# Kernel optimization log

Hardware: AMD Instinct MI355X
Metric: run time of the kernel (lower is better)

## Reference

```python
import jax, jax.numpy as jnp
import numpy as np
from jax import lax

BATCH, HID = 8192, 512


def setup_inputs() -> dict:
    key = jax.random.key(0)
    ks = jax.random.split(key, 9)
    s = 0.05
    return {
        "h": jax.random.normal(ks[0], (BATCH, HID), jnp.float32),
        "W1": jax.random.normal(ks[1], (2 * HID, HID), jnp.float32) * s,
        "b1": jax.random.normal(ks[2], (2 * HID,), jnp.float32) * s,
        "W2": jax.random.normal(ks[3], (2 * HID, 2 * HID), jnp.float32) * s,
        "b2": jax.random.normal(ks[4], (2 * HID,), jnp.float32) * s,
        "W3": jax.random.normal(ks[5], (HID, 2 * HID), jnp.float32) * s,
        "b3": jax.random.normal(ks[6], (HID,), jnp.float32) * s,
        "Wt": jax.random.normal(ks[7], (HID, 1), jnp.float32) * s,
        "bt": jax.random.normal(ks[8], (HID,), jnp.float32) * s,
        "n_steps": 10,
    }


def reference(h, W1, b1, W2, b2, W3, b3, Wt, bt, n_steps):
    dt = 1.0 / n_steps  # t_span = (0, 1)

    def ode_func(t, hh):
        # time_embed(Linear(1,H)) on a column of t's: t * Wt[:,0] + bt
        t_emb = t * Wt[:, 0] + bt                      # (H,), broadcast over batch
        x = hh + t_emb                                 # (B, H)
        x = jnp.tanh(x @ W1.T + b1)                    # (B, 2H)
        x = jnp.tanh(x @ W2.T + b2)                    # (B, 2H)
        return x @ W3.T + b3                           # (B, H)

    def rk4_step(hh, t):
        k1 = ode_func(t, hh)
        k2 = ode_func(t + dt / 2, hh + dt / 2 * k1)
        k3 = ode_func(t + dt / 2, hh + dt / 2 * k2)
        k4 = ode_func(t + dt, hh + dt * k3)
        return hh + dt / 6 * (k1 + 2 * k2 + 2 * k3 + k4), None

    ts = (jnp.arange(n_steps, dtype=h.dtype) * dt)     # step start times
    h_out, _ = lax.scan(rk4_step, h, ts)
    return h_out
```

## Files before the change

### kernel.cpp

```cpp
#include <hip/hip_runtime.h>
#include <hip/hip_bf16.h>
#include <math.h>
#include <stdint.h>

using bf16 = __hip_bfloat16;
typedef __attribute__((ext_vector_type(8))) short short8;
typedef __attribute__((ext_vector_type(4))) float floatx4;
typedef __attribute__((ext_vector_type(4))) int int4v;

typedef const __attribute__((address_space(1))) void* gptr_t;
typedef __attribute__((address_space(3))) void* lptr_t;

__device__ __forceinline__ void load_lds16(const void* g, void* l) {
    __builtin_amdgcn_global_load_lds((gptr_t)(uintptr_t)g, (lptr_t)(uintptr_t)l, 16, 0, 0);
}

#define WAIT_VM(n) __builtin_amdgcn_s_waitcnt(0x0F70 | ((n) & 15) | (((n) >> 4) << 14))

__device__ __forceinline__ float fast_tanh(float x) {
    float e = __expf(2.f * x);
    return 1.f - 2.f / (e + 1.f);
}


__global__ void __launch_bounds__(256, 2)
gemm_tanh4(const bf16* __restrict__ A, const bf16* __restrict__ W,
           const float* __restrict__ bias, int8_t* __restrict__ out,
           int K, int N) {
    constexpr int MT = 4, NT = 4;
    __shared__ alignas(16) bf16 lA[2][128 * 64];
    __shared__ alignas(16) bf16 lB[2][128 * 64];

    const int b   = blockIdx.x + gridDim.x * blockIdx.y;
    const int xcd = b & 7, j = b >> 3;
    const int bx  = j & 7;
    const int by  = xcd + 8 * (j >> 3);

    const int tid  = threadIdx.x;
    const int lane = tid & 63;
    const int w    = tid >> 6;
    const int wr   = w >> 1, wc = w & 1;
    const int quad = lane >> 4, l16 = lane & 15;
    const int brow = by * 128;
    const int bcol = bx * 128;

    const bf16* gA[4]; const bf16* gW[4]; int lq[4];
#pragma unroll
    for (int jj = 0; jj < 4; ++jj) {
        const int q = tid + jj * 256;
        const int r = q >> 3, s = (q & 7) ^ (r & 7);
        gA[jj] = A + (size_t)(brow + r) * K + s * 8;
        gW[jj] = W + (size_t)(bcol + r) * K + s * 8;
        lq[jj] = q * 8;
    }

    floatx4 acc[MT][NT];
    const floatx4 zero = {0.f, 0.f, 0.f, 0.f};
#pragma unroll
    for (int mt = 0; mt < MT; ++mt)
#pragma unroll
        for (int nt = 0; nt < NT; ++nt) acc[mt][nt] = zero;

    const int arow0 = wr * 64 + l16;
    const int brow0 = wc * 64 + l16;
    const int x7 = l16 & 7;

    const int nIter = K / 64;
#pragma unroll
    for (int jj = 0; jj < 4; ++jj) load_lds16(gA[jj], &lA[0][0] + lq[jj]);
#pragma unroll
    for (int jj = 0; jj < 4; ++jj) load_lds16(gW[jj], &lB[0][0] + lq[jj]);

    for (int kt = 0; kt < nIter; ++kt) {
        const int cur = kt & 1;
        if (kt + 1 < nIter) {
#pragma unroll
            for (int jj = 0; jj < 4; ++jj)
                load_lds16(gA[jj] + (kt + 1) * 64, &lA[cur ^ 1][0] + lq[jj]);
#pragma unroll
            for (int jj = 0; jj < 4; ++jj)
                load_lds16(gW[jj] + (kt + 1) * 64, &lB[cur ^ 1][0] + lq[jj]);
            WAIT_VM(8);
        } else {
            WAIT_VM(0);
        }
        __builtin_amdgcn_s_barrier();

#pragma unroll
        for (int kk = 0; kk < 2; ++kk) {
            const int sw = ((kk * 4 + quad) ^ x7) * 8;
            short8 af[MT], bfr[NT];
#pragma unroll
            for (int mt = 0; mt < MT; ++mt)
                af[mt] = *(const short8*)(&lA[cur][0] + (arow0 + mt * 16) * 64 + sw);
#pragma unroll
            for (int nt = 0; nt < NT; ++nt)
                bfr[nt] = *(const short8*)(&lB[cur][0] + (brow0 + nt * 16) * 64 + sw);
#pragma unroll
            for (int mt = 0; mt < MT; ++mt)
#pragma unroll
                for (int nt = 0; nt < NT; ++nt)
                    acc[mt][nt] = __builtin_amdgcn_mfma_f32_16x16x32_bf16(
                        af[mt], bfr[nt], acc[mt][nt], 0, 0, 0);
        }
        __builtin_amdgcn_s_barrier();
    }

    const int m0 = brow + wr * 64 + quad * 4;
    const int n0 = bcol + wc * 64 + l16;
#pragma unroll
    for (int mt = 0; mt < MT; ++mt)
#pragma unroll
        for (int nt = 0; nt < NT; ++nt) {
            const int n = n0 + nt * 16;
            const float bb = bias[n];
#pragma unroll
            for (int i = 0; i < 4; ++i) {
                const int m = m0 + mt * 16 + i;
                const float t = fast_tanh(acc[mt][nt][i] + bb);
                out[(size_t)m * N + n] = (int8_t)__float2int_rn(t * 127.f);
            }
        }
}

__global__ void __launch_bounds__(256, 2)
gemm_tanh_i8(const int8_t* __restrict__ A, const int8_t* __restrict__ W,
             const float* __restrict__ dq, const float* __restrict__ bias,
             int8_t* __restrict__ out, int K, int N) {
    constexpr int MT = 4, NT = 4;
    __shared__ alignas(16) int8_t lA[2][128 * 128];
    __shared__ alignas(16) int8_t lB[2][128 * 128];

    const int b   = blockIdx.x + gridDim.x * blockIdx.y;
    const int xcd = b & 7, j = b >> 3;
    const int bx  = j & 7;
    const int by  = xcd + 8 * (j >> 3);

    const int tid  = threadIdx.x;
    const int lane = tid & 63;
    const int w    = tid >> 6;
    const int wr   = w >> 1, wc = w & 1;
    const int quad = lane >> 4, l16 = lane & 15;
    const int brow = by * 128;
    const int bcol = bx * 128;

    const int8_t* gA[4]; const int8_t* gW[4]; int lq[4];
#pragma unroll
    for (int jj = 0; jj < 4; ++jj) {
        const int q = tid + jj * 256;
        const int r = q >> 3, s = (q & 7) ^ (r & 7);
        gA[jj] = A + (size_t)(brow + r) * K + s * 16;
        gW[jj] = W + (size_t)(bcol + r) * K + s * 16;
        lq[jj] = q * 16;
    }

    int4v acc[MT][NT];
    const int4v izero = {0, 0, 0, 0};
#pragma unroll
    for (int mt = 0; mt < MT; ++mt)
#pragma unroll
        for (int nt = 0; nt < NT; ++nt) acc[mt][nt] = izero;

    const int arow0 = wr * 64 + l16;
    const int brow0 = wc * 64 + l16;
    const int x7 = l16 & 7;

    const int nIter = K / 128;
#pragma unroll
    for (int jj = 0; jj < 4; ++jj) load_lds16(gA[jj], &lA[0][0] + lq[jj]);
#pragma unroll
    for (int jj = 0; jj < 4; ++jj) load_lds16(gW[jj], &lB[0][0] + lq[jj]);

    for (int kt = 0; kt < nIter; ++kt) {
        const int cur = kt & 1;
        if (kt + 1 < nIter) {
#pragma unroll
            for (int jj = 0; jj < 4; ++jj)
                load_lds16(gA[jj] + (kt + 1) * 128, &lA[cur ^ 1][0] + lq[jj]);
#pragma unroll
            for (int jj = 0; jj < 4; ++jj)
                load_lds16(gW[jj] + (kt + 1) * 128, &lB[cur ^ 1][0] + lq[jj]);
            WAIT_VM(8);
        } else {
            WAIT_VM(0);
        }
        __builtin_amdgcn_s_barrier();

#pragma unroll
        for (int kk = 0; kk < 2; ++kk) {
            const int sw = ((kk * 4 + quad) ^ x7) * 16;
            int4v af[MT], bfr[NT];
#pragma unroll
            for (int mt = 0; mt < MT; ++mt)
                af[mt] = *(const int4v*)(&lA[cur][(arow0 + mt * 16) * 128 + sw]);
#pragma unroll
            for (int nt = 0; nt < NT; ++nt)
                bfr[nt] = *(const int4v*)(&lB[cur][(brow0 + nt * 16) * 128 + sw]);
#pragma unroll
            for (int mt = 0; mt < MT; ++mt)
#pragma unroll
                for (int nt = 0; nt < NT; ++nt)
                    acc[mt][nt] = __builtin_amdgcn_mfma_i32_16x16x64_i8(
                        af[mt], bfr[nt], acc[mt][nt], 0, 0, 0);
        }
        __builtin_amdgcn_s_barrier();
    }

    const int m0 = brow + wr * 64 + quad * 4;
    const int n0 = bcol + wc * 64 + l16;
#pragma unroll
    for (int mt = 0; mt < MT; ++mt)
#pragma unroll
        for (int nt = 0; nt < NT; ++nt) {
            const int n = n0 + nt * 16;
            const float bb = bias[n];
            const float dqn = dq[n];
#pragma unroll
            for (int i = 0; i < 4; ++i) {
                const int m = m0 + mt * 16 + i;
                const float t = fast_tanh((float)acc[mt][nt][i] * dqn + bb);
                out[(size_t)m * N + n] = (int8_t)__float2int_rn(t * 127.f);
            }
        }
}

__global__ void __launch_bounds__(256, 2)
gemm_k(const int8_t* __restrict__ A, const int8_t* __restrict__ W,
       const float* __restrict__ dq, const float* __restrict__ bias, int K,
       bf16* __restrict__ kacc, const bf16* __restrict__ hb_src,
       const float* __restrict__ h_src, float* __restrict__ h_out,
       bf16* __restrict__ hb_out, bf16* __restrict__ x0_out,
       const float* __restrict__ temb, float alpha, float dt6, int mode) {
    constexpr int MT = 4, NT = 2;
    __shared__ alignas(16) int8_t lA[2][128 * 128];
    __shared__ alignas(16) int8_t lB[2][64 * 128];

    const int b   = blockIdx.x + gridDim.x * blockIdx.y;
    const int xcd = b & 7, j = b >> 3;
    const int bx  = j & 7;
    const int by  = xcd + 8 * (j >> 3);

    const int tid  = threadIdx.x;
    const int lane = tid & 63;
    const int w    = tid >> 6;
    const int wr   = w >> 1, wc = w & 1;
    const int quad = lane >> 4, l16 = lane & 15;
    const int brow = by * 128;
    const int bcol = bx * 64;

    const int8_t* gA[4]; int lqA[4];
    const int8_t* gW[2]; int lqB[2];
#pragma unroll
    for (int jj = 0; jj < 4; ++jj) {
        const int q = tid + jj * 256;
        const int r = q >> 3, s = (q & 7) ^ (r & 7);
        gA[jj]  = A + (size_t)(brow + r) * K + s * 16;
        lqA[jj] = q * 16;
    }
#pragma unroll
    for (int jj = 0; jj < 2; ++jj) {
        const int q = tid + jj * 256;
        const int r = q >> 3, s = (q & 7) ^ (r & 7);
        gW[jj]  = W + (size_t)(bcol + r) * K + s * 16;
        lqB[jj] = q * 16;
    }

    int4v acc[MT][NT];
    const int4v izero = {0, 0, 0, 0};
#pragma unroll
    for (int mt = 0; mt < MT; ++mt)
#pragma unroll
        for (int nt = 0; nt < NT; ++nt) acc[mt][nt] = izero;

    const int arow0 = wr * 64 + l16;
    const int brow0 = wc * 32 + l16;
    const int x7 = l16 & 7;

    const int nIter = K / 128;
#pragma unroll
    for (int jj = 0; jj < 4; ++jj) load_lds16(gA[jj], &lA[0][0] + lqA[jj]);
#pragma unroll
    for (int jj = 0; jj < 2; ++jj) load_lds16(gW[jj], &lB[0][0] + lqB[jj]);

    for (int kt = 0; kt < nIter; ++kt) {
        const int cur = kt & 1;
        if (kt + 1 < nIter) {
#pragma unroll
            for (int jj = 0; jj < 4; ++jj)
                load_lds16(gA[jj] + (kt + 1) * 128, &lA[cur ^ 1][0] + lqA[jj]);
#pragma unroll
            for (int jj = 0; jj < 2; ++jj)
                load_lds16(gW[jj] + (kt + 1) * 128, &lB[cur ^ 1][0] + lqB[jj]);
            WAIT_VM(6);
        } else {
            WAIT_VM(0);
        }
        __builtin_amdgcn_s_barrier();

#pragma unroll
        for (int kk = 0; kk < 2; ++kk) {
            const int sw = ((kk * 4 + quad) ^ x7) * 16;
            int4v af[MT], bfr[NT];
#pragma unroll
            for (int mt = 0; mt < MT; ++mt)
                af[mt] = *(const int4v*)(&lA[cur][(arow0 + mt * 16) * 128 + sw]);
#pragma unroll
            for (int nt = 0; nt < NT; ++nt)
                bfr[nt] = *(const int4v*)(&lB[cur][(brow0 + nt * 16) * 128 + sw]);
#pragma unroll
            for (int mt = 0; mt < MT; ++mt)
#pragma unroll
                for (int nt = 0; nt < NT; ++nt)
                    acc[mt][nt] = __builtin_amdgcn_mfma_i32_16x16x64_i8(
                        af[mt], bfr[nt], acc[mt][nt], 0, 0, 0);
        }
        __builtin_amdgcn_s_barrier();
    }

    const int m0 = brow + wr * 64 + quad * 4;
    const int n0 = bcol + wc * 32 + l16;
#pragma unroll
    for (int mt = 0; mt < MT; ++mt)
#pragma unroll
        for (int nt = 0; nt < NT; ++nt) {
            const int n = n0 + nt * 16;
            const float bb = bias[n];
            const float dqn = dq[n];
            const float te = temb[n];
#pragma unroll
            for (int i = 0; i < 4; ++i) {
                const int m = m0 + mt * 16 + i;
                const size_t idx = (size_t)m * 512 + n;
                const float kv = (float)acc[mt][nt][i] * dqn + bb;
                if (mode == 0) {
                    kacc[idx] = __float2bfloat16(kv);
                    x0_out[idx] = __float2bfloat16(
                        __bfloat162float(hb_src[idx]) + alpha * kv + te);
                } else if (mode == 1) {
                    kacc[idx] = __float2bfloat16(__bfloat162float(kacc[idx]) + 2.f * kv);
                    x0_out[idx] = __float2bfloat16(
                        __bfloat162float(hb_src[idx]) + alpha * kv + te);
                } else {
                    const float hn = h_src[idx] + dt6 * (__bfloat162float(kacc[idx]) + kv);
                    h_out[idx] = hn;
                    hb_out[idx] = __float2bfloat16(hn);
                    if (x0_out) x0_out[idx] = __float2bfloat16(hn + te);
                }
            }
        }
}

__global__ void f2b_kern(const float* __restrict__ src, bf16* __restrict__ dst, int n) {
    const int i = blockIdx.x * blockDim.x + threadIdx.x;
    if (i < n) dst[i] = __float2bfloat16(src[i]);
}

__global__ void quantW_row(const float* __restrict__ W, int K,
                           int8_t* __restrict__ out, float* __restrict__ dq) {
    __shared__ float red[256];
    const int row = blockIdx.x, tid = threadIdx.x;
    const float* src = W + (size_t)row * K;
    float m = 0.f;
    for (int k = tid; k < K; k += 256) m = fmaxf(m, fabsf(src[k]));
    red[tid] = m;
    __syncthreads();
    for (int s = 128; s > 0; s >>= 1) {
        if (tid < s) red[tid] = fmaxf(red[tid], red[tid + s]);
        __syncthreads();
    }
    const float rmax = fmaxf(red[0], 1e-8f);
    const float sc = 127.f / rmax;
    int8_t* dst = out + (size_t)row * K;
    for (int k = tid; k < K; k += 256) {
        int v = __float2int_rn(src[k] * sc);
        v = v > 127 ? 127 : (v < -127 ? -127 : v);
        dst[k] = (int8_t)v;
    }
    if (tid == 0) dq[row] = rmax / (127.f * 127.f);
}

__global__ void temb_kern(const float* __restrict__ Wt, const float* __restrict__ bt,
                          float* __restrict__ temb, float half_dt, int total) {
    const int i = blockIdx.x * blockDim.x + threadIdx.x;
    if (i < total) {
        const int j = i >> 9, n = i & 511;
        temb[i] = (j * half_dt) * Wt[n] + bt[n];
    }
}

__global__ void prep_kern(const float* __restrict__ h, const float* __restrict__ temb0,
                          bf16* __restrict__ x0, bf16* __restrict__ hb, int total) {
    const int i = blockIdx.x * blockDim.x + threadIdx.x;
    if (i < total) {
        const float hv = h[i];
        x0[i] = __float2bfloat16(hv + temb0[i & 511]);
        hb[i] = __float2bfloat16(hv);
    }
}

extern "C" void kernel_launch(void* const* d_in, const int* in_sizes, int n_in,
                              void* d_out, int out_size, void* d_ws, size_t ws_size,
                              hipStream_t stream) {
    const float* h_in = (const float*)d_in[0];
    const float* W1 = (const float*)d_in[1];
    const float* b1 = (const float*)d_in[2];
    const float* W2 = (const float*)d_in[3];
    const float* b2 = (const float*)d_in[4];
    const float* W3 = (const float*)d_in[5];
    const float* b3 = (const float*)d_in[6];
    const float* Wt = (const float*)d_in[7];
    const float* bt = (const float*)d_in[8];
    const int B = 8192, H = 512, H2 = 1024, NS = 10;
    const float dt = 1.f / NS;

    char* ws = (char*)d_ws;
    auto alloc = [&](size_t bytes) {
        char* p = ws;
        ws += (bytes + 255) & ~(size_t)255;
        return p;
    };
    bf16* W1b = (bf16*)alloc((size_t)H2 * H * 2);
    int8_t* W2i = (int8_t*)alloc((size_t)H2 * H2);
    float* dq2  = (float*)alloc((size_t)H2 * 4);
    int8_t* W3i = (int8_t*)alloc((size_t)H * H2);
    float* dq3  = (float*)alloc((size_t)H * 4);
    bf16* x0b = (bf16*)alloc((size_t)B * H * 2);
    int8_t* x1i = (int8_t*)alloc((size_t)B * H2);
    int8_t* x2i = (int8_t*)alloc((size_t)B * H2);
    bf16* kacc = (bf16*)alloc((size_t)B * H * 2);
    bf16* hb   = (bf16*)alloc((size_t)B * H * 2);
    float* temb = (float*)alloc((size_t)21 * H * 4);
    float* hbuf = (float*)d_out;

    {
        int n = H2 * H;
        f2b_kern<<<(n + 255) / 256, 256, 0, stream>>>(W1, W1b, n);
        quantW_row<<<H2, 256, 0, stream>>>(W2, H2, W2i, dq2);
        quantW_row<<<H, 256, 0, stream>>>(W3, H2, W3i, dq3);
    }
    {
        const int total = 21 * H;
        temb_kern<<<(total + 255) / 256, 256, 0, stream>>>(Wt, bt, temb, dt * 0.5f, total);
    }
    {
        const int total = B * H;
        prep_kern<<<(total + 255) / 256, 256, 0, stream>>>(h_in, temb, x0b, hb, total);
    }

    const dim3 blk256(256);
    const dim3 g12(H2 / 128, B / 128);
    const dim3 g3(H / 64, B / 128);

    for (int s = 0; s < NS; ++s) {
        const float* hs = (s == 0) ? h_in : hbuf;
        const float* tmid = temb + (size_t)(2 * s + 1) * H;
        const float* tend = temb + (size_t)(2 * s + 2) * H;
        for (int e = 0; e < 4; ++e) {
            gemm_tanh4<<<g12, blk256, 0, stream>>>(x0b, W1b, b1, x1i, H, H2);
            gemm_tanh_i8<<<g12, blk256, 0, stream>>>(x1i, W2i, dq2, b2, x2i, H2, H2);
            if (e == 0)
                gemm_k<<<g3, blk256, 0, stream>>>(x2i, W3i, dq3, b3, H2, kacc, hb, hs,
                                                  nullptr, nullptr, x0b, tmid,
                                                  dt * 0.5f, 0.f, 0);
            else if (e == 1)
                gemm_k<<<g3, blk256, 0, stream>>>(x2i, W3i, dq3, b3, H2, kacc, hb, hs,
                                                  nullptr, nullptr, x0b, tmid,
                                                  dt * 0.5f, 0.f, 1);
            else if (e == 2)
                gemm_k<<<g3, blk256, 0, stream>>>(x2i, W3i, dq3, b3, H2, kacc, hb, hs,
                                                  nullptr, nullptr, x0b, tend,
                                                  dt, 0.f, 1);
            else
                gemm_k<<<g3, blk256, 0, stream>>>(x2i, W3i, dq3, b3, H2, kacc, hb, hs,
                                                  hbuf, hb,
                                                  (s == NS - 1) ? nullptr : x0b,
                                                  tend, 0.f, dt / 6.f, 2);
        }
    }
}
```

Measured before the change: 2.103 ms.

## Fold W3 into W1 and track pre-activation h·W1 across RK4 stages

The change precomputes W13 = W1·W3 and folds the time embedding and the biases into per-stage constant tables. It then keeps h·W1ᵀ as a float state, so each RK4 stage is an int8 layer-2 GEMM followed by a fused W13 GEMM that directly produces the next layer-1 activation. The separate layer-1 GEMM per stage and the bf16 state round-trips go away. The k accumulation is kept as int16 sums of quantized tanh outputs, and one combined update GEMM advances both hW1 and h. The cost is extra float hW1 traffic, and numerical error rises from int8 quantization of the composed W13 and from the k-average being quantized to int8.

```diff
diff --git a/kernel.cpp b/kernel.cpp
--- a/kernel.cpp
+++ b/kernel.cpp
@@ -24,9 +24,9 @@
 
 
 __global__ void __launch_bounds__(256, 2)
-gemm_tanh4(const bf16* __restrict__ A, const bf16* __restrict__ W,
-           const float* __restrict__ bias, int8_t* __restrict__ out,
-           int K, int N) {
+gemm_init(const bf16* __restrict__ A, const bf16* __restrict__ W,
+          const float* __restrict__ c0n, float* __restrict__ hW1,
+          int8_t* __restrict__ x1q, int K) {
     constexpr int MT = 4, NT = 4;
     __shared__ alignas(16) bf16 lA[2][128 * 64];
     __shared__ alignas(16) bf16 lB[2][128 * 64];
@@ -113,21 +113,24 @@
 #pragma unroll
         for (int nt = 0; nt < NT; ++nt) {
             const int n = n0 + nt * 16;
-            const float bb = bias[n];
+            const float cn = c0n[n];
 #pragma unroll
             for (int i = 0; i < 4; ++i) {
                 const int m = m0 + mt * 16 + i;
-                const float t = fast_tanh(acc[mt][nt][i] + bb);
-                out[(size_t)m * N + n] = (int8_t)__float2int_rn(t * 127.f);
+                const size_t idx = (size_t)m * 1024 + n;
+                const float v = acc[mt][nt][i];
+                hW1[idx] = v;
+                x1q[idx] = (int8_t)__float2int_rn(127.f * fast_tanh(v + cn));
             }
         }
 }
 
 __global__ void __launch_bounds__(256, 2)
-gemm_tanh_i8(const int8_t* __restrict__ A, const int8_t* __restrict__ W,
-             const float* __restrict__ dq, const float* __restrict__ bias,
-             int8_t* __restrict__ out, int K, int N) {
-    constexpr int MT = 4, NT = 4;
+gemm_l2(const int8_t* __restrict__ A, const int8_t* __restrict__ W,
+        const float* __restrict__ dq, const float* __restrict__ bias,
+        int8_t* __restrict__ x2q, int16_t* __restrict__ xacc16,
+        int8_t* __restrict__ xaccq, int mode) {
+    constexpr int MT = 4, NT = 4, K = 1024;
     __shared__ alignas(16) int8_t lA[2][128 * 128];
     __shared__ alignas(16) int8_t lB[2][128 * 128];
 
@@ -218,22 +221,30 @@
 #pragma unroll
             for (int i = 0; i < 4; ++i) {
                 const int m = m0 + mt * 16 + i;
-                const float t = fast_tanh((float)acc[mt][nt][i] * dqn + bb);
-                out[(size_t)m * N + n] = (int8_t)__float2int_rn(t * 127.f);
+                const size_t idx = (size_t)m * 1024 + n;
+                const int q = __float2int_rn(
+                    127.f * fast_tanh((float)acc[mt][nt][i] * dqn + bb));
+                if (mode == 0) {
+                    x2q[idx] = (int8_t)q;
+                    xacc16[idx] = (int16_t)q;
+                } else if (mode == 1) {
+                    x2q[idx] = (int8_t)q;
+                    xacc16[idx] = (int16_t)(xacc16[idx] + 2 * q);
+                } else {
+                    const int tot = (int)xacc16[idx] + q;
+                    xaccq[idx] = (int8_t)__float2int_rn((float)tot * (1.f / 6.f));
+                }
             }
         }
 }
 
 __global__ void __launch_bounds__(256, 2)
-gemm_k(const int8_t* __restrict__ A, const int8_t* __restrict__ W,
-       const float* __restrict__ dq, const float* __restrict__ bias, int K,
-       bf16* __restrict__ kacc, const bf16* __restrict__ hb_src,
-       const float* __restrict__ h_src, float* __restrict__ h_out,
-       bf16* __restrict__ hb_out, bf16* __restrict__ x0_out,
-       const float* __restrict__ temb, float alpha, float dt6, int mode) {
-    constexpr int MT = 4, NT = 2;
+gemm_u(const int8_t* __restrict__ A, const int8_t* __restrict__ W,
+       const float* __restrict__ dq, const float* __restrict__ hW1,
+       const float* __restrict__ c, float alpha, int8_t* __restrict__ x1q) {
+    constexpr int MT = 4, NT = 4, K = 1024;
     __shared__ alignas(16) int8_t lA[2][128 * 128];
-    __shared__ alignas(16) int8_t lB[2][64 * 128];
+    __shared__ alignas(16) int8_t lB[2][128 * 128];
 
     const int b   = blockIdx.x + gridDim.x * blockIdx.y;
     const int xcd = b & 7, j = b >> 3;
@@ -246,23 +257,16 @@
     const int wr   = w >> 1, wc = w & 1;
     const int quad = lane >> 4, l16 = lane & 15;
     const int brow = by * 128;
-    const int bcol = bx * 64;
-
-    const int8_t* gA[4]; int lqA[4];
-    const int8_t* gW[2]; int lqB[2];
+    const int bcol = bx * 128;
+
+    const int8_t* gA[4]; const int8_t* gW[4]; int lq[4];
 #pragma unroll
     for (int jj = 0; jj < 4; ++jj) {
         const int q = tid + jj * 256;
         const int r = q >> 3, s = (q & 7) ^ (r & 7);
-        gA[jj]  = A + (size_t)(brow + r) * K + s * 16;
-        lqA[jj] = q * 16;
-    }
-#pragma unroll
-    for (int jj = 0; jj < 2; ++jj) {
-        const int q = tid + jj * 256;
-        const int r = q >> 3, s = (q & 7) ^ (r & 7);
-        gW[jj]  = W + (size_t)(bcol + r) * K + s * 16;
-        lqB[jj] = q * 16;
+        gA[jj] = A + (size_t)(brow + r) * K + s * 16;
+        gW[jj] = W + (size_t)(bcol + r) * K + s * 16;
+        lq[jj] = q * 16;
     }
 
     int4v acc[MT][NT];
@@ -273,25 +277,25 @@
         for (int nt = 0; nt < NT; ++nt) acc[mt][nt] = izero;
 
     const int arow0 = wr * 64 + l16;
-    const int brow0 = wc * 32 + l16;
+    const int brow0 = wc * 64 + l16;
     const int x7 = l16 & 7;
 
     const int nIter = K / 128;
 #pragma unroll
-    for (int jj = 0; jj < 4; ++jj) load_lds16(gA[jj], &lA[0][0] + lqA[jj]);
-#pragma unroll
-    for (int jj = 0; jj < 2; ++jj) load_lds16(gW[jj], &lB[0][0] + lqB[jj]);
+    for (int jj = 0; jj < 4; ++jj) load_lds16(gA[jj], &lA[0][0] + lq[jj]);
+#pragma unroll
+    for (int jj = 0; jj < 4; ++jj) load_lds16(gW[jj], &lB[0][0] + lq[jj]);
 
     for (int kt = 0; kt < nIter; ++kt) {
         const int cur = kt & 1;
         if (kt + 1 < nIter) {
 #pragma unroll
             for (int jj = 0; jj < 4; ++jj)
-                load_lds16(gA[jj] + (kt + 1) * 128, &lA[cur ^ 1][0] + lqA[jj]);
-#pragma unroll
-            for (int jj = 0; jj < 2; ++jj)
-                load_lds16(gW[jj] + (kt + 1) * 128, &lB[cur ^ 1][0] + lqB[jj]);
-            WAIT_VM(6);
+                load_lds16(gA[jj] + (kt + 1) * 128, &lA[cur ^ 1][0] + lq[jj]);
+#pragma unroll
+            for (int jj = 0; jj < 4; ++jj)
+                load_lds16(gW[jj] + (kt + 1) * 128, &lB[cur ^ 1][0] + lq[jj]);
+            WAIT_VM(8);
         } else {
             WAIT_VM(0);
         }
@@ -318,41 +322,164 @@
     }
 
     const int m0 = brow + wr * 64 + quad * 4;
-    const int n0 = bcol + wc * 32 + l16;
+    const int n0 = bcol + wc * 64 + l16;
 #pragma unroll
     for (int mt = 0; mt < MT; ++mt)
 #pragma unroll
         for (int nt = 0; nt < NT; ++nt) {
             const int n = n0 + nt * 16;
-            const float bb = bias[n];
-            const float dqn = dq[n];
-            const float te = temb[n];
+            const float dqa = dq[n] * alpha;
+            const float cn = c[n];
 #pragma unroll
             for (int i = 0; i < 4; ++i) {
                 const int m = m0 + mt * 16 + i;
-                const size_t idx = (size_t)m * 512 + n;
-                const float kv = (float)acc[mt][nt][i] * dqn + bb;
-                if (mode == 0) {
-                    kacc[idx] = __float2bfloat16(kv);
-                    x0_out[idx] = __float2bfloat16(
-                        __bfloat162float(hb_src[idx]) + alpha * kv + te);
-                } else if (mode == 1) {
-                    kacc[idx] = __float2bfloat16(__bfloat162float(kacc[idx]) + 2.f * kv);
-                    x0_out[idx] = __float2bfloat16(
-                        __bfloat162float(hb_src[idx]) + alpha * kv + te);
+                const size_t idx = (size_t)m * 1024 + n;
+                const float u = hW1[idx] + dqa * (float)acc[mt][nt][i] + cn;
+                x1q[idx] = (int8_t)__float2int_rn(127.f * fast_tanh(u));
+            }
+        }
+}
+
+__global__ void __launch_bounds__(256, 2)
+gemm_upd(const int8_t* __restrict__ A, const int8_t* __restrict__ W,
+         const float* __restrict__ dq, const float* __restrict__ updc,
+         float dtv, float* __restrict__ hW1, const float* __restrict__ c0n,
+         int8_t* __restrict__ x1q, const float* __restrict__ hsrc,
+         float* __restrict__ hdst, int last, int bxoff) {
+    constexpr int MT = 4, NT = 4, K = 1024;
+    __shared__ alignas(16) int8_t lA[2][128 * 128];
+    __shared__ alignas(16) int8_t lB[2][128 * 128];
+
+    const int bx = blockIdx.x + bxoff;
+    const int by = blockIdx.y;
+
+    const int tid  = threadIdx.x;
+    const int lane = tid & 63;
+    const int w    = tid >> 6;
+    const int wr   = w >> 1, wc = w & 1;
+    const int quad = lane >> 4, l16 = lane & 15;
+    const int brow = by * 128;
+    const int bcol = bx * 128;
+
+    const int8_t* gA[4]; const int8_t* gW[4]; int lq[4];
+#pragma unroll
+    for (int jj = 0; jj < 4; ++jj) {
+        const int q = tid + jj * 256;
+        const int r = q >> 3, s = (q & 7) ^ (r & 7);
+        gA[jj] = A + (size_t)(brow + r) * K + s * 16;
+        gW[jj] = W + (size_t)(bcol + r) * K + s * 16;
+        lq[jj] = q * 16;
+    }
+
+    int4v acc[MT][NT];
+    const int4v izero = {0, 0, 0, 0};
+#pragma unroll
+    for (int mt = 0; mt < MT; ++mt)
+#pragma unroll
+        for (int nt = 0; nt < NT; ++nt) acc[mt][nt] = izero;
+
+    const int arow0 = wr * 64 + l16;
+    const int brow0 = wc * 64 + l16;
+    const int x7 = l16 & 7;
+
+    const int nIter = K / 128;
+#pragma unroll
+    for (int jj = 0; jj < 4; ++jj) load_lds16(gA[jj], &lA[0][0] + lq[jj]);
+#pragma unroll
+    for (int jj = 0; jj < 4; ++jj) load_lds16(gW[jj], &lB[0][0] + lq[jj]);
+
+    for (int kt = 0; kt < nIter; ++kt) {
+        const int cur = kt & 1;
+        if (kt + 1 < nIter) {
+#pragma unroll
+            for (int jj = 0; jj < 4; ++jj)
+                load_lds16(gA[jj] + (kt + 1) * 128, &lA[cur ^ 1][0] + lq[jj]);
+#pragma unroll
+            for (int jj = 0; jj < 4; ++jj)
+                load_lds16(gW[jj] + (kt + 1) * 128, &lB[cur ^ 1][0] + lq[jj]);
+            WAIT_VM(8);
+        } else {
+            WAIT_VM(0);
+        }
+        __builtin_amdgcn_s_barrier();
+
+#pragma unroll
+        for (int kk = 0; kk < 2; ++kk) {
+            const int sw = ((kk * 4 + quad) ^ x7) * 16;
+            int4v af[MT], bfr[NT];
+#pragma unroll
+            for (int mt = 0; mt < MT; ++mt)
+                af[mt] = *(const int4v*)(&lA[cur][(arow0 + mt * 16) * 128 + sw]);
+#pragma unroll
+            for (int nt = 0; nt < NT; ++nt)
+                bfr[nt] = *(const int4v*)(&lB[cur][(brow0 + nt * 16) * 128 + sw]);
+#pragma unroll
+            for (int mt = 0; mt < MT; ++mt)
+#pragma unroll
+                for (int nt = 0; nt < NT; ++nt)
+                    acc[mt][nt] = __builtin_amdgcn_mfma_i32_16x16x64_i8(
+                        af[mt], bfr[nt], acc[mt][nt], 0, 0, 0);
+        }
+        __builtin_amdgcn_s_barrier();
+    }
+
+    const int m0 = brow + wr * 64 + quad * 4;
+    const int n0 = bcol + wc * 64 + l16;
+#pragma unroll
+    for (int mt = 0; mt < MT; ++mt)
+#pragma unroll
+        for (int nt = 0; nt < NT; ++nt) {
+            const int n = n0 + nt * 16;
+            const float dqn = dq[n] * dtv;
+            const float uc = updc[n];
+#pragma unroll
+            for (int i = 0; i < 4; ++i) {
+                const int m = m0 + mt * 16 + i;
+                const float add = dqn * (float)acc[mt][nt][i] + uc;
+                if (n < 1024) {
+                    if (!last) {
+                        const size_t idx = (size_t)m * 1024 + n;
+                        const float v = hW1[idx] + add;
+                        hW1[idx] = v;
+                        x1q[idx] = (int8_t)__float2int_rn(
+                            127.f * fast_tanh(v + c0n[n]));
+                    }
                 } else {
-                    const float hn = h_src[idx] + dt6 * (__bfloat162float(kacc[idx]) + kv);
-                    h_out[idx] = hn;
-                    hb_out[idx] = __float2bfloat16(hn);
-                    if (x0_out) x0_out[idx] = __float2bfloat16(hn + te);
+                    const size_t idx2 = (size_t)m * 512 + (n - 1024);
+                    hdst[idx2] = hsrc[idx2] + add;
                 }
             }
         }
 }
+
 
 __global__ void f2b_kern(const float* __restrict__ src, bf16* __restrict__ dst, int n) {
     const int i = blockIdx.x * blockDim.x + threadIdx.x;
     if (i < n) dst[i] = __float2bfloat16(src[i]);
+}
+
+__global__ void tr_kern(const float* __restrict__ W3, float* __restrict__ W3T) {
+    const int i = blockIdx.x * blockDim.x + threadIdx.x;
+    if (i < 1024 * 512) {
+        const int jq = i >> 9, k = i & 511;
+        W3T[i] = W3[(size_t)k * 1024 + jq];
+    }
+}
+
+__global__ void w13_kern(const float* __restrict__ W1, const float* __restrict__ W3T,
+                         float* __restrict__ W13) {
+    const int tid = threadIdx.x;
+    const int ti = tid >> 4, tj = tid & 15;
+    const int i = blockIdx.y * 16 + ti;
+    const int jq = blockIdx.x * 16 + tj;
+    const float4* a = (const float4*)(W1 + (size_t)i * 512);
+    const float4* bv = (const float4*)(W3T + (size_t)jq * 512);
+    float acc = 0.f;
+    for (int k = 0; k < 128; ++k) {
+        const float4 av = a[k], bw = bv[k];
+        acc += av.x * bw.x + av.y * bw.y + av.z * bw.z + av.w * bw.w;
+    }
+    W13[(size_t)i * 1024 + jq] = acc;
 }
 
 __global__ void quantW_row(const float* __restrict__ W, int K,
@@ -379,22 +506,47 @@
     if (tid == 0) dq[row] = rmax / (127.f * 127.f);
 }
 
-__global__ void temb_kern(const float* __restrict__ Wt, const float* __restrict__ bt,
-                          float* __restrict__ temb, float half_dt, int total) {
+__global__ void cwv_kern(const float* __restrict__ W1, const float* __restrict__ Wt,
+                         const float* __restrict__ bt, const float* __restrict__ b3,
+                         float* __restrict__ WtW1, float* __restrict__ btW1,
+                         float* __restrict__ b3W1) {
+    const int i = blockIdx.x, l = threadIdx.x;
+    float a = 0.f, bb = 0.f, c = 0.f;
+    for (int k = l; k < 512; k += 64) {
+        const float wv = W1[(size_t)i * 512 + k];
+        a += wv * Wt[k];
+        bb += wv * bt[k];
+        c += wv * b3[k];
+    }
+    for (int off = 32; off > 0; off >>= 1) {
+        a += __shfl_down(a, off);
+        bb += __shfl_down(bb, off);
+        c += __shfl_down(c, off);
+    }
+    if (l == 0) { WtW1[i] = a; btW1[i] = bb; b3W1[i] = c; }
+}
+
+__global__ void ctab_kern(const float* __restrict__ WtW1, const float* __restrict__ btW1,
+                          const float* __restrict__ b3W1, const float* __restrict__ b1,
+                          const float* __restrict__ b3,
+                          float* __restrict__ c0, float* __restrict__ cmid,
+                          float* __restrict__ cend, float* __restrict__ updc, float dt) {
     const int i = blockIdx.x * blockDim.x + threadIdx.x;
-    if (i < total) {
-        const int j = i >> 9, n = i & 511;
-        temb[i] = (j * half_dt) * Wt[n] + bt[n];
-    }
-}
-
-__global__ void prep_kern(const float* __restrict__ h, const float* __restrict__ temb0,
-                          bf16* __restrict__ x0, bf16* __restrict__ hb, int total) {
-    const int i = blockIdx.x * blockDim.x + threadIdx.x;
-    if (i < total) {
-        const float hv = h[i];
-        x0[i] = __float2bfloat16(hv + temb0[i & 511]);
-        hb[i] = __float2bfloat16(hv);
+    const float hd = dt * 0.5f;
+    if (i < 11 * 1024) {
+        const int s = i >> 10, n = i & 1023;
+        c0[i] = (2 * s) * hd * WtW1[n] + btW1[n] + b1[n];
+    } else if (i < 21 * 1024) {
+        const int t = i - 11 * 1024;
+        const int s = t >> 10, n = t & 1023;
+        cmid[t] = (2 * s + 1) * hd * WtW1[n] + btW1[n] + b1[n] + hd * b3W1[n];
+    } else if (i < 31 * 1024) {
+        const int t = i - 21 * 1024;
+        const int s = t >> 10, n = t & 1023;
+        cend[t] = (2 * s + 2) * hd * WtW1[n] + btW1[n] + b1[n] + dt * b3W1[n];
+    } else if (i < 31 * 1024 + 1536) {
+        const int n = i - 31 * 1024;
+        updc[n] = (n < 1024) ? dt * b3W1[n] : dt * b3[n - 1024];
     }
 }
 
@@ -419,62 +571,65 @@
         ws += (bytes + 255) & ~(size_t)255;
         return p;
     };
-    bf16* W1b = (bf16*)alloc((size_t)H2 * H * 2);
-    int8_t* W2i = (int8_t*)alloc((size_t)H2 * H2);
-    float* dq2  = (float*)alloc((size_t)H2 * 4);
-    int8_t* W3i = (int8_t*)alloc((size_t)H * H2);
-    float* dq3  = (float*)alloc((size_t)H * 4);
-    bf16* x0b = (bf16*)alloc((size_t)B * H * 2);
-    int8_t* x1i = (int8_t*)alloc((size_t)B * H2);
-    int8_t* x2i = (int8_t*)alloc((size_t)B * H2);
-    bf16* kacc = (bf16*)alloc((size_t)B * H * 2);
-    bf16* hb   = (bf16*)alloc((size_t)B * H * 2);
-    float* temb = (float*)alloc((size_t)21 * H * 4);
-    float* hbuf = (float*)d_out;
-
-    {
-        int n = H2 * H;
-        f2b_kern<<<(n + 255) / 256, 256, 0, stream>>>(W1, W1b, n);
-        quantW_row<<<H2, 256, 0, stream>>>(W2, H2, W2i, dq2);
-        quantW_row<<<H, 256, 0, stream>>>(W3, H2, W3i, dq3);
-    }
-    {
-        const int total = 21 * H;
-        temb_kern<<<(total + 255) / 256, 256, 0, stream>>>(Wt, bt, temb, dt * 0.5f, total);
-    }
-    {
-        const int total = B * H;
-        prep_kern<<<(total + 255) / 256, 256, 0, stream>>>(h_in, temb, x0b, hb, total);
-    }
+    bf16*   W1b    = (bf16*)alloc((size_t)H2 * H * 2);
+    int8_t* W2i    = (int8_t*)alloc((size_t)H2 * H2);
+    float*  dq2    = (float*)alloc((size_t)H2 * 4);
+    int8_t* Wupd   = (int8_t*)alloc((size_t)1536 * H2);
+    float*  dqupd  = (float*)alloc((size_t)1536 * 4);
+    float*  WtW1   = (float*)alloc((size_t)H2 * 4);
+    float*  btW1   = (float*)alloc((size_t)H2 * 4);
+    float*  b3W1   = (float*)alloc((size_t)H2 * 4);
+    float*  c0t    = (float*)alloc((size_t)11 * H2 * 4);
+    float*  cmid   = (float*)alloc((size_t)10 * H2 * 4);
+    float*  cend   = (float*)alloc((size_t)10 * H2 * 4);
+    float*  updc   = (float*)alloc((size_t)1536 * 4);
+    float*  hW1    = (float*)alloc((size_t)B * H2 * 4);
+    int8_t* x1q    = (int8_t*)alloc((size_t)B * H2);
+    int8_t* x2q    = (int8_t*)alloc((size_t)B * H2);
+    int16_t* xacc16 = (int16_t*)alloc((size_t)B * H2 * 2);
+    int8_t* xaccq  = (int8_t*)alloc((size_t)B * H2);
+    float*  hbuf   = (float*)d_out;
+
+    bf16*  hbf  = (bf16*)x2q;
+    float* W13f = (float*)xacc16;
+    float* W3T  = (float*)(xacc16 + (size_t)B * H2 / 2);
+
+    f2b_kern<<<(H2 * H + 255) / 256, 256, 0, stream>>>(W1, W1b, H2 * H);
+    f2b_kern<<<(B * H + 255) / 256, 256, 0, stream>>>(h_in, hbf, B * H);
+    tr_kern<<<(H2 * H + 255) / 256, 256, 0, stream>>>(W3, W3T);
+    w13_kern<<<dim3(64, 64), 256, 0, stream>>>(W1, W3T, W13f);
+    quantW_row<<<H2, 256, 0, stream>>>(W13f, H2, Wupd, dqupd);
+    quantW_row<<<H, 256, 0, stream>>>(W3, H2, Wupd + (size_t)H2 * H2, dqupd + H2);
+    quantW_row<<<H2, 256, 0, stream>>>(W2, H2, W2i, dq2);
+    cwv_kern<<<H2, 64, 0, stream>>>(W1, Wt, bt, b3, WtW1, btW1, b3W1);
+    ctab_kern<<<(31 * 1024 + 1536 + 255) / 256, 256, 0, stream>>>(
+        WtW1, btW1, b3W1, b1, b3, c0t, cmid, cend, updc, dt);
 
     const dim3 blk256(256);
-    const dim3 g12(H2 / 128, B / 128);
-    const dim3 g3(H / 64, B / 128);
+    const dim3 g(8, 64);
+
+    gemm_init<<<g, blk256, 0, stream>>>(hbf, W1b, c0t, hW1, x1q, H);
 
     for (int s = 0; s < NS; ++s) {
+        const float* cm = cmid + (size_t)s * H2;
+        const float* ce = cend + (size_t)s * H2;
+        const int last = (s == NS - 1) ? 1 : 0;
+        gemm_l2<<<g, blk256, 0, stream>>>(x1q, W2i, dq2, b2, x2q, xacc16, xaccq, 0);
+        gemm_u<<<g, blk256, 0, stream>>>(x2q, Wupd, dqupd, hW1, cm, dt * 0.5f, x1q);
+        gemm_l2<<<g, blk256, 0, stream>>>(x1q, W2i, dq2, b2, x2q, xacc16, xaccq, 1);
+        gemm_u<<<g, blk256, 0, stream>>>(x2q, Wupd, dqupd, hW1, cm, dt * 0.5f, x1q);
+        gemm_l2<<<g, blk256, 0, stream>>>(x1q, W2i, dq2, b2, x2q, xacc16, xaccq, 1);
+        gemm_u<<<g, blk256, 0, stream>>>(x2q, Wupd, dqupd, hW1, ce, dt, x1q);
+        gemm_l2<<<g, blk256, 0, stream>>>(x1q, W2i, dq2, b2, x2q, xacc16, xaccq, 2);
         const float* hs = (s == 0) ? h_in : hbuf;
-        const float* tmid = temb + (size_t)(2 * s + 1) * H;
-        const float* tend = temb + (size_t)(2 * s + 2) * H;
-        for (int e = 0; e < 4; ++e) {
-            gemm_tanh4<<<g12, blk256, 0, stream>>>(x0b, W1b, b1, x1i, H, H2);
-            gemm_tanh_i8<<<g12, blk256, 0, stream>>>(x1i, W2i, dq2, b2, x2i, H2, H2);
-            if (e == 0)
-                gemm_k<<<g3, blk256, 0, stream>>>(x2i, W3i, dq3, b3, H2, kacc, hb, hs,
-                                                  nullptr, nullptr, x0b, tmid,
-                                                  dt * 0.5f, 0.f, 0);
-            else if (e == 1)
-                gemm_k<<<g3, blk256, 0, stream>>>(x2i, W3i, dq3, b3, H2, kacc, hb, hs,
-                                                  nullptr, nullptr, x0b, tmid,
-                                                  dt * 0.5f, 0.f, 1);
-            else if (e == 2)
-                gemm_k<<<g3, blk256, 0, stream>>>(x2i, W3i, dq3, b3, H2, kacc, hb, hs,
-                                                  nullptr, nullptr, x0b, tend,
-                                                  dt, 0.f, 1);
-            else
-                gemm_k<<<g3, blk256, 0, stream>>>(x2i, W3i, dq3, b3, H2, kacc, hb, hs,
-                                                  hbuf, hb,
-                                                  (s == NS - 1) ? nullptr : x0b,
-                                                  tend, 0.f, dt / 6.f, 2);
-        }
-    }
-}
+        if (!last) {
+            gemm_upd<<<dim3(12, 64), blk256, 0, stream>>>(
+                xaccq, Wupd, dqupd, updc, dt, hW1,
+                c0t + (size_t)(s + 1) * H2, x1q, hs, hbuf, 0, 0);
+        } else {
+            gemm_upd<<<dim3(4, 64), blk256, 0, stream>>>(
+                xaccq, Wupd, dqupd, updc, dt, hW1,
+                c0t + (size_t)(s + 1) * H2, x1q, hs, hbuf, 1, 8);
+        }
+    }
+}
```

Result: slower. 2.636 ms (+25.3%).
